# Performance work log

Hardware: AMD Instinct MI355X
Metric: run time of the kernel (lower is better)

## Reference

```python
import jax, jax.numpy as jnp
import numpy as np

N = 100000   # nodes
E = 1600000  # edges (avg degree 16)
IN, HID, OUT = 128, 128, 64
EPS = 1e-5


def setup_inputs() -> dict:
    key = jax.random.key(0)
    ks = jax.random.split(key, 8)
    x = jax.random.normal(ks[0], (N, IN), dtype=jnp.float32)
    edge_index = jax.random.randint(ks[1], (2, E), 0, N, dtype=jnp.int64)

    def w(k, i, o):
        return jax.random.normal(k, (i, o), dtype=jnp.float32) / np.float32(np.sqrt(i))

    return {
        'x': x,
        'edge_index': edge_index,
        'W1': w(ks[2], IN, HID), 'b1': jnp.zeros((HID,), jnp.float32),
        'g1': jnp.ones((HID,), jnp.float32), 'be1': jnp.zeros((HID,), jnp.float32),
        'W2': w(ks[3], HID, HID), 'b2': jnp.zeros((HID,), jnp.float32),
        'g2': jnp.ones((HID,), jnp.float32), 'be2': jnp.zeros((HID,), jnp.float32),
        'W3': w(ks[4], HID, OUT), 'b3': jnp.zeros((OUT,), jnp.float32),
    }


def gcn_conv(x, W, b, src, dst, n):
    # GCNConv: x' = D^{-1/2} (A + I) D^{-1/2} X W + b
    h = x @ W                                   # [N, F_out]
    loop = jnp.arange(n, dtype=src.dtype)
    s = jnp.concatenate([src, loop])            # self-loops appended
    d = jnp.concatenate([dst, loop])
    deg = jax.ops.segment_sum(jnp.ones_like(d, dtype=h.dtype), d, num_segments=n)
    dinv = jax.lax.rsqrt(jnp.maximum(deg, 1.0))  # deg >= 1 due to self-loops
    norm = dinv[s] * dinv[d]                     # [E+N]
    out = jax.ops.segment_sum(h[s] * norm[:, None], d, num_segments=n)
    return out + b


def batch_norm(x, gamma, beta):
    m = x.mean(axis=0)
    v = x.var(axis=0)  # biased variance, as used for normalization in torch BN
    return (x - m) * jax.lax.rsqrt(v + EPS) * gamma + beta


def reference(x, edge_index, W1, b1, g1, be1, W2, b2, g2, be2, W3, b3):
    src, dst = edge_index[0], edge_index[1]
    r = x                                        # residual (skip = Identity, in_dim == hidden_dim)
    h = batch_norm(gcn_conv(x, W1, b1, src, dst, N), g1, be1) + r
    r = h
    h = jax.nn.relu(h)                           # dropout p=0 -> identity
    h = batch_norm(gcn_conv(h, W2, b2, src, dst, N), g2, be2) + r
    h = jax.nn.relu(h)
    out = gcn_conv(h, W3, b3, src, dst, N)       # last layer: no bn/skip/relu
    return out
```

## Files before the change

### kernel.cpp

```cpp
#include <hip/hip_runtime.h>

static constexpr int kN = 100000;
static constexpr int kE = 1600000;
static constexpr float kEps = 1e-5f;

static constexpr int kBSH = 9;
static constexpr int kNB = (kN + 511) >> kBSH;
static constexpr int kBCAP = 12288;
static constexpr int kCHUNK = 4096;
static constexpr int kPad = 16;

typedef __attribute__((ext_vector_type(8))) short short8;
typedef __attribute__((ext_vector_type(4))) float float4v;
typedef __attribute__((ext_vector_type(2))) float float2v;

static __device__ inline unsigned short f2bf(float f) {
  union { float f; unsigned int u; } v; v.f = f;
  unsigned int r = v.u + 0x7fffu + ((v.u >> 16) & 1u);
  return (unsigned short)(r >> 16);
}
static __device__ inline float bf2f(unsigned int bits16) {
  union { unsigned int u; float f; } v; v.u = bits16 << 16; return v.f;
}
static __device__ inline unsigned int pack2bf(float lo, float hi) {
  return (unsigned int)f2bf(lo) | ((unsigned int)f2bf(hi) << 16);
}

__global__ __launch_bounds__(512) void bin_k(const int* __restrict__ src,
                                             const int* __restrict__ dst,
                                             int* __restrict__ gcursor,
                                             int2* __restrict__ gstage) {
  __shared__ int s_cnt[256];
  __shared__ int s_scan[256];
  __shared__ int s_base[256];
  __shared__ int s_cur[256];
  __shared__ int s_gb[256];
  __shared__ int2 s_stage[kCHUNK];
  int tid = threadIdx.x;
  int e0 = blockIdx.x * kCHUNK;
  int n = kE - e0; if (n > kCHUNK) n = kCHUNK;
  if (tid < 256) s_cnt[tid] = 0;
  __syncthreads();
  for (int j = tid; j < n; j += 512) {
    atomicAdd(&s_cnt[dst[e0 + j] >> kBSH], 1);
  }
  __syncthreads();
  int v = 0;
  if (tid < 256) { v = s_cnt[tid]; s_scan[tid] = v; }
  __syncthreads();
  #pragma unroll
  for (int o = 1; o < 256; o <<= 1) {
    int t = (tid >= o && tid < 256) ? s_scan[tid - o] : 0;
    __syncthreads();
    if (tid < 256) s_scan[tid] += t;
    __syncthreads();
  }
  if (tid < 256) {
    int excl = s_scan[tid] - v;
    s_base[tid] = excl;
    s_cur[tid] = excl;
  }
  __syncthreads();
  if (tid < kNB && s_cnt[tid] > 0) s_gb[tid] = atomicAdd(&gcursor[tid], s_cnt[tid]);
  for (int j = tid; j < n; j += 512) {
    int s = src[e0 + j];
    int d = dst[e0 + j];
    int p = atomicAdd(&s_cur[d >> kBSH], 1);
    s_stage[p] = make_int2(s, d);
  }
  __syncthreads();
  for (int j = tid; j < n; j += 512) {
    int2 e = s_stage[j];
    int b = e.y >> kBSH;
    gstage[(size_t)b * kBCAP + s_gb[b] + (j - s_base[b])] = e;
  }
}

__global__ __launch_bounds__(256) void alloc_hist_k(const int2* __restrict__ gstage,
                                                    const int* __restrict__ gcursor,
                                                    int* __restrict__ counter,
                                                    int* __restrict__ deg,
                                                    int* __restrict__ row_start,
                                                    float* __restrict__ dinv) {
  __shared__ int s_deg[1 << kBSH];
  __shared__ int s_scan[256];
  __shared__ int s_bcast;
  int b = blockIdx.x, tid = threadIdx.x;
  int n0 = b << kBSH;
  s_deg[tid] = 0;
  s_deg[tid + 256] = 0;
  __syncthreads();
  int cnt = gcursor[b];
  const int2* seg = gstage + (size_t)b * kBCAP;
  for (int j = tid; j < cnt; j += 256) {
    atomicAdd(&s_deg[seg[j].y - n0], 1);
  }
  __syncthreads();
  int i0 = 2 * tid, i1 = 2 * tid + 1;
  int d0 = s_deg[i0], d1 = s_deg[i1];
  int pd0 = (d0 + kPad - 1) & ~(kPad - 1);
  int pd1 = (d1 + kPad - 1) & ~(kPad - 1);
  int sum = pd0 + pd1;
  s_scan[tid] = sum;
  __syncthreads();
  #pragma unroll
  for (int o = 1; o < 256; o <<= 1) {
    int t = (tid >= o) ? s_scan[tid - o] : 0;
    __syncthreads();
    s_scan[tid] += t;
    __syncthreads();
  }
  if (tid == 255) s_bcast = atomicAdd(counter, s_scan[255]);
  __syncthreads();
  int base = s_bcast + s_scan[tid] - sum;
  int node0 = n0 + i0, node1 = n0 + i1;
  if (node0 < kN) {
    deg[node0] = d0;
    row_start[node0] = base;
    dinv[node0] = rsqrtf((float)(d0 + 1));
  }
  if (node1 < kN) {
    deg[node1] = d1;
    row_start[node1] = base + pd0;
    dinv[node1] = rsqrtf((float)(d1 + 1));
  }
}

__global__ __launch_bounds__(256) void scatter2_k(const int2* __restrict__ gstage,
                                                  const int* __restrict__ gcursor,
                                                  const int* __restrict__ rowst,
                                                  const int* __restrict__ deg,
                                                  int* __restrict__ csr_src) {
  __shared__ int s_cur[1 << kBSH];
  int b = blockIdx.x, tid = threadIdx.x;
  int n0 = b << kBSH;
  int nn = kN - n0; if (nn > (1 << kBSH)) nn = 1 << kBSH;
  for (int i = tid; i < nn; i += 256) s_cur[i] = rowst[n0 + i];
  __syncthreads();
  int cnt = gcursor[b];
  const int2* seg = gstage + (size_t)b * kBCAP;
  for (int j = tid; j < cnt; j += 256) {
    int2 e = seg[j];
    int pos = atomicAdd(&s_cur[e.y - n0], 1);
    csr_src[pos] = e.x;
  }
  __syncthreads();
  for (int i = tid; i < nn; i += 256) {
    int d = deg[n0 + i];
    int endp = rowst[n0 + i] + ((d + kPad - 1) & ~(kPad - 1));
    for (int p = s_cur[i]; p < endp; ++p) csr_src[p] = kN;
  }
}

__global__ void convert_w_all_k(const float* __restrict__ W1, const float* __restrict__ W2,
                                const float* __restrict__ W3,
                                unsigned short* __restrict__ wf1,
                                unsigned short* __restrict__ wf2,
                                unsigned short* __restrict__ wf3,
                                unsigned char* __restrict__ hF8,
                                unsigned short* __restrict__ hH,
                                float* __restrict__ stats) {
  int tid = blockIdx.x * blockDim.x + threadIdx.x;
  const float* W;
  unsigned short* Wf;
  int BNO;
  if (tid < 2048) { W = W1; Wf = wf1; BNO = 128; }
  else if (tid < 4096) { W = W2; Wf = wf2; BNO = 128; tid -= 2048; }
  else if (tid < 5120) { W = W3; Wf = wf3; BNO = 64; tid -= 4096; }
  else if (tid < 5152) {
    ((unsigned int*)(hF8 + (size_t)kN * 128))[tid - 5120] = 0u;
    return;
  } else if (tid < 5184) {
    ((unsigned int*)(hH + (size_t)kN * 64))[tid - 5152] = 0u;
    return;
  } else if (tid < 5696) {
    stats[tid - 5184] = 0.f;
    return;
  } else return;
  int l = tid & 63;
  int frag = tid >> 6;
  int q = frag & 3;
  int t = frag >> 2;
  int n = t * 16 + (l & 15);
  int kbase = q * 32 + ((l >> 4) << 3);
  unsigned short v[8] __attribute__((aligned(16)));
  #pragma unroll
  for (int j = 0; j < 8; ++j) v[j] = f2bf(W[(kbase + j) * BNO + n]);
  ((uint4*)Wf)[tid] = *(const uint4*)v;
}

template <int BNO, int AMODE, bool OUT8>
__global__ __launch_bounds__(256) void gemm_mfma_k(const void* __restrict__ Aptr,
                                                   const void* __restrict__ Rptr,
                                                   const float* __restrict__ stats,
                                                   const float* __restrict__ g,
                                                   const float* __restrict__ be,
                                                   unsigned int* __restrict__ Zptr,
                                                   const unsigned short* __restrict__ Wf,
                                                   const float* __restrict__ dinv,
                                                   void* __restrict__ Cptr) {
  __shared__ float lss[256];
  if constexpr (AMODE != 0) {
    int t = threadIdx.x;
    if (t < 128) {
      float mean = stats[t] * (1.f / kN);
      float var = stats[128 + t] * (1.f / kN) - mean * mean;
      float inv = rsqrtf(var + kEps);
      float sc = g[t] * inv;
      lss[t] = sc;
      lss[128 + t] = be[t] - mean * sc;
    }
    __syncthreads();
  }
  int wid = (int)((blockIdx.x * blockDim.x + threadIdx.x) >> 6);
  if (wid >= kN / 16) return;
  int l = threadIdx.x & 63;
  int r0 = wid * 16;
  short8 a[4];
  if constexpr (AMODE == 0) {
    const float* Af = (const float*)Aptr + (size_t)(r0 + (l & 15)) * 128 + ((l >> 4) << 3);
    #pragma unroll
    for (int q = 0; q < 4; ++q) {
      float4 u0 = *(const float4*)(Af + q * 32);
      float4 u1 = *(const float4*)(Af + q * 32 + 4);
      short8 t;
      t[0] = (short)f2bf(u0.x); t[1] = (short)f2bf(u0.y);
      t[2] = (short)f2bf(u0.z); t[3] = (short)f2bf(u0.w);
      t[4] = (short)f2bf(u1.x); t[5] = (short)f2bf(u1.y);
      t[6] = (short)f2bf(u1.z); t[7] = (short)f2bf(u1.w);
      a[q] = t;
    }
  } else {
    int row = r0 + (l & 15);
    int cg0 = l >> 4;
    const uint4* Ab = (const uint4*)Aptr + (size_t)row * 16;
    #pragma unroll
    for (int q = 0; q < 4; ++q) {
      int cg = q * 4 + cg0;
      int c0 = cg * 8;
      uint4 av = Ab[cg];
      float r[8];
      if constexpr (AMODE == 1) {
        const float4* Rf = (const float4*)Rptr + (size_t)row * 32 + cg * 2;
        float4 r0v = Rf[0], r1v = Rf[1];
        r[0] = r0v.x; r[1] = r0v.y; r[2] = r0v.z; r[3] = r0v.w;
        r[4] = r1v.x; r[5] = r1v.y; r[6] = r1v.z; r[7] = r1v.w;
      } else {
        uint4 rv = ((const uint4*)Rptr)[(size_t)row * 16 + cg];
        r[0] = bf2f(rv.x & 0xffffu); r[1] = bf2f(rv.x >> 16);
        r[2] = bf2f(rv.y & 0xffffu); r[3] = bf2f(rv.y >> 16);
        r[4] = bf2f(rv.z & 0xffffu); r[5] = bf2f(rv.z >> 16);
        r[6] = bf2f(rv.w & 0xffffu); r[7] = bf2f(rv.w >> 16);
      }
      unsigned int apk[4] = {av.x, av.y, av.z, av.w};
      float o[8];
      #pragma unroll
      for (int j = 0; j < 4; ++j) {
        o[2 * j]     = lss[c0 + 2 * j] * bf2f(apk[j] & 0xffffu) + lss[128 + c0 + 2 * j] + r[2 * j];
        o[2 * j + 1] = lss[c0 + 2 * j + 1] * bf2f(apk[j] >> 16) + lss[128 + c0 + 2 * j + 1] + r[2 * j + 1];
      }
      if constexpr (AMODE == 1) {
        uint4 zv;
        zv.x = pack2bf(o[0], o[1]); zv.y = pack2bf(o[2], o[3]);
        zv.z = pack2bf(o[4], o[5]); zv.w = pack2bf(o[6], o[7]);
        ((uint4*)Zptr)[(size_t)row * 16 + cg] = zv;
      }
      short8 t;
      #pragma unroll
      for (int j = 0; j < 8; ++j) t[j] = (short)f2bf(fmaxf(o[j], 0.f));
      a[q] = t;
    }
  }
  const short8* Wv = (const short8*)Wf + l;
  constexpr int NT = BNO / 16;
  float4v acc[NT];
  #pragma unroll
  for (int t = 0; t < NT; ++t) {
    acc[t] = (float4v){0.f, 0.f, 0.f, 0.f};
    #pragma unroll
    for (int q = 0; q < 4; ++q) {
      short8 b = Wv[(t * 4 + q) * 64];
      acc[t] = __builtin_amdgcn_mfma_f32_16x16x32_bf16(a[q], b, acc[t], 0, 0, 0);
    }
  }
  int orow = r0 + ((l >> 4) << 2);
  int ocol = l & 15;
  float dv[4];
  #pragma unroll
  for (int r = 0; r < 4; ++r) dv[r] = dinv[orow + r];
  #pragma unroll
  for (int t = 0; t < NT; ++t) {
    #pragma unroll
    for (int r = 0; r < 4; ++r) {
      float val = acc[t][r] * dv[r];
      if constexpr (OUT8) {
        unsigned int u = __builtin_amdgcn_cvt_pk_fp8_f32(val, val, 0u, false);
        ((unsigned char*)Cptr)[(size_t)(orow + r) * BNO + t * 16 + ocol] = (unsigned char)(u & 0xffu);
      } else {
        ((unsigned short*)Cptr)[(size_t)(orow + r) * BNO + t * 16 + ocol] = f2bf(val);
      }
    }
  }
}

__global__ __launch_bounds__(256) void aggregate128_k(
    const unsigned char* __restrict__ H8, const int* __restrict__ row_start,
    const int* __restrict__ deg, const int* __restrict__ csr_src,
    const float* __restrict__ dinv, const float* __restrict__ bias,
    unsigned int* __restrict__ outp, float* __restrict__ stats) {
  __shared__ float s_sum[128], s_sq[128];
  int tid = threadIdx.x;
  if (tid < 128) { s_sum[tid] = 0.f; s_sq[tid] = 0.f; }
  __syncthreads();
  int lane = tid & 63;
  int qt = lane >> 4;
  int ql = lane & 15;
  int nwaves = gridDim.x * (blockDim.x >> 6);
  int gwave = (int)((blockIdx.x * blockDim.x + tid) >> 6);
  const uint2* H2 = (const uint2*)H8;
  float4 blo = ((const float4*)bias)[2 * ql];
  float4 bhi = ((const float4*)bias)[2 * ql + 1];
  float st[8] = {0.f, 0.f, 0.f, 0.f, 0.f, 0.f, 0.f, 0.f};
  float sqa[8] = {0.f, 0.f, 0.f, 0.f, 0.f, 0.f, 0.f, 0.f};
  auto accum = [](float (&a)[8], uint2 v) {
    float2v p0 = __builtin_amdgcn_cvt_pk_f32_fp8(v.x, false);
    float2v p1 = __builtin_amdgcn_cvt_pk_f32_fp8(v.x, true);
    float2v p2 = __builtin_amdgcn_cvt_pk_f32_fp8(v.y, false);
    float2v p3 = __builtin_amdgcn_cvt_pk_f32_fp8(v.y, true);
    a[0] += p0.x; a[1] += p0.y; a[2] += p1.x; a[3] += p1.y;
    a[4] += p2.x; a[5] += p2.y; a[6] += p3.x; a[7] += p3.y;
  };
  int node = gwave;
  int rs = 0, pd = 0;
  float di = 1.f;
  int ec = kN;
  if (node < kN) {
    rs = row_start[node];
    pd = (deg[node] + kPad - 1) & ~(kPad - 1);
    di = dinv[node];
    ec = csr_src[rs + lane];
  }
  while (node < kN) {
    int cur_rs = rs, cur_pd = pd, cur_e = ec;
    float cur_di = di;
    int nxt = node + nwaves;
    if (nxt < kN) {
      rs = row_start[nxt];
      pd = (deg[nxt] + kPad - 1) & ~(kPad - 1);
      di = dinv[nxt];
      ec = csr_src[rs + lane];
    }
    float a[8] = {0.f, 0.f, 0.f, 0.f, 0.f, 0.f, 0.f, 0.f};
    uint2 vself = H2[(size_t)node * 16 + ql];
    int nb = cur_pd >> 4;
    int nb4 = nb > 4 ? 4 : nb;
    for (int i = 0; i < nb4; ++i) {
      int s[4];
      uint2 v[4];
      #pragma unroll
      for (int j = 0; j < 4; ++j) s[j] = __shfl(cur_e, i * 16 + 4 * j + qt, 64);
      #pragma unroll
      for (int j = 0; j < 4; ++j) v[j] = H2[(size_t)s[j] * 16 + ql];
      #pragma unroll
      for (int j = 0; j < 4; ++j) accum(a, v[j]);
    }
    for (int i = 4; i < nb; ++i) {
      int ee = csr_src[cur_rs + i * 16 + (lane & 15)];
      int s[4];
      uint2 v[4];
      #pragma unroll
      for (int j = 0; j < 4; ++j) s[j] = __shfl(ee, 4 * j + qt, 64);
      #pragma unroll
      for (int j = 0; j < 4; ++j) v[j] = H2[(size_t)s[j] * 16 + ql];
      #pragma unroll
      for (int j = 0; j < 4; ++j) accum(a, v[j]);
    }
    #pragma unroll
    for (int j = 0; j < 8; ++j) {
      a[j] += __shfl_xor(a[j], 16, 64);
      a[j] += __shfl_xor(a[j], 32, 64);
    }
    accum(a, vself);
    if (qt == 0) {
      float o[8];
      o[0] = cur_di * a[0] + blo.x; o[1] = cur_di * a[1] + blo.y;
      o[2] = cur_di * a[2] + blo.z; o[3] = cur_di * a[3] + blo.w;
      o[4] = cur_di * a[4] + bhi.x; o[5] = cur_di * a[5] + bhi.y;
      o[6] = cur_di * a[6] + bhi.z; o[7] = cur_di * a[7] + bhi.w;
      uint4 ov;
      ov.x = pack2bf(o[0], o[1]); ov.y = pack2bf(o[2], o[3]);
      ov.z = pack2bf(o[4], o[5]); ov.w = pack2bf(o[6], o[7]);
      ((uint4*)outp)[(size_t)node * 16 + ql] = ov;
      #pragma unroll
      for (int j = 0; j < 8; ++j) { st[j] += o[j]; sqa[j] += o[j] * o[j]; }
    }
    node = nxt;
  }
  if (qt == 0) {
    #pragma unroll
    for (int j = 0; j < 8; ++j) {
      atomicAdd(&s_sum[8 * ql + j], st[j]);
      atomicAdd(&s_sq[8 * ql + j], sqa[j]);
    }
  }
  __syncthreads();
  if (tid < 128) {
    atomicAdd(&stats[tid], s_sum[tid]);
    atomicAdd(&stats[128 + tid], s_sq[tid]);
  }
}

__global__ __launch_bounds__(256) void aggregate64_k(
    const unsigned short* __restrict__ Hb, const int* __restrict__ row_start,
    const int* __restrict__ deg, const int* __restrict__ csr_src,
    const float* __restrict__ dinv, const float* __restrict__ bias,
    float* __restrict__ outp) {
  int tid = threadIdx.x;
  int lane = tid & 63;
  int qt = lane >> 4;
  int ql = lane & 15;
  int nwaves = gridDim.x * (blockDim.x >> 6);
  int gwave = (int)((blockIdx.x * blockDim.x + tid) >> 6);
  const uint2* H2 = (const uint2*)Hb;
  float4 b4 = ((const float4*)bias)[ql];
  auto accum = [](float (&a)[4], uint2 v) {
    a[0] += bf2f(v.x & 0xffffu); a[1] += bf2f(v.x >> 16);
    a[2] += bf2f(v.y & 0xffffu); a[3] += bf2f(v.y >> 16);
  };
  int node = gwave;
  int rs = 0, pd = 0;
  float di = 1.f;
  int ec = kN;
  if (node < kN) {
    rs = row_start[node];
    pd = (deg[node] + kPad - 1) & ~(kPad - 1);
    di = dinv[node];
    ec = csr_src[rs + lane];
  }
  while (node < kN) {
    int cur_rs = rs, cur_pd = pd, cur_e = ec;
    float cur_di = di;
    int nxt = node + nwaves;
    if (nxt < kN) {
      rs = row_start[nxt];
      pd = (deg[nxt] + kPad - 1) & ~(kPad - 1);
      di = dinv[nxt];
      ec = csr_src[rs + lane];
    }
    float a[4] = {0.f, 0.f, 0.f, 0.f};
    uint2 vself = H2[(size_t)node * 16 + ql];
    int nb = cur_pd >> 4;
    int nb4 = nb > 4 ? 4 : nb;
    for (int i = 0; i < nb4; ++i) {
      int s[4];
      uint2 v[4];
      #pragma unroll
      for (int j = 0; j < 4; ++j) s[j] = __shfl(cur_e, i * 16 + 4 * j + qt, 64);
      #pragma unroll
      for (int j = 0; j < 4; ++j) v[j] = H2[(size_t)s[j] * 16 + ql];
      #pragma unroll
      for (int j = 0; j < 4; ++j) accum(a, v[j]);
    }
    for (int i = 4; i < nb; ++i) {
      int ee = csr_src[cur_rs + i * 16 + (lane & 15)];
      int s[4];
      uint2 v[4];
      #pragma unroll
      for (int j = 0; j < 4; ++j) s[j] = __shfl(ee, 4 * j + qt, 64);
      #pragma unroll
      for (int j = 0; j < 4; ++j) v[j] = H2[(size_t)s[j] * 16 + ql];
      #pragma unroll
      for (int j = 0; j < 4; ++j) accum(a, v[j]);
    }
    #pragma unroll
    for (int j = 0; j < 4; ++j) {
      a[j] += __shfl_xor(a[j], 16, 64);
      a[j] += __shfl_xor(a[j], 32, 64);
    }
    accum(a, vself);
    if (qt == 0) {
      ((float4*)outp)[(size_t)node * 16 + ql] =
          make_float4(cur_di * a[0] + b4.x, cur_di * a[1] + b4.y,
                      cur_di * a[2] + b4.z, cur_di * a[3] + b4.w);
    }
    node = nxt;
  }
}

extern "C" void kernel_launch(void* const* d_in, const int* in_sizes, int n_in,
                              void* d_out, int out_size, void* d_ws, size_t ws_size,
                              hipStream_t stream) {
  const float* x   = (const float*)d_in[0];
  const int*   ei  = (const int*)d_in[1];
  const float* W1  = (const float*)d_in[2];
  const float* b1  = (const float*)d_in[3];
  const float* g1  = (const float*)d_in[4];
  const float* be1 = (const float*)d_in[5];
  const float* W2  = (const float*)d_in[6];
  const float* b2  = (const float*)d_in[7];
  const float* g2  = (const float*)d_in[8];
  const float* be2 = (const float*)d_in[9];
  const float* W3  = (const float*)d_in[10];
  const float* b3  = (const float*)d_in[11];
  float* outp = (float*)d_out;

  const int* src = ei;
  const int* dst = ei + kE;

  char* ws = (char*)d_ws;
  size_t off = 0;
  auto alloc = [&](size_t bytes) -> void* {
    void* p = ws + off;
    off = (off + bytes + 255) & ~size_t(255);
    return p;
  };
  unsigned char* hF8 = (unsigned char*)alloc((size_t)(kN + 1) * 128);
  unsigned short* hH = (unsigned short*)alloc((size_t)(kN + 1) * 64 * 2);
  unsigned int* aB = (unsigned int*)alloc((size_t)kN * 64 * 4);
  unsigned int* zC = (unsigned int*)alloc((size_t)kN * 64 * 4);
  int*   csr_src  = (int*)alloc((size_t)(3200000 + 64) * 4);
  int2*  gstage   = (int2*)alloc((size_t)kNB * kBCAP * 8);
  int*   gcursor  = (int*)alloc((kNB + 1) * 4);
  int*   counter  = gcursor + kNB;
  int*   deg      = (int*)alloc((size_t)kN * 4);
  float* dinv     = (float*)alloc((size_t)kN * 4);
  int*   rowst    = (int*)alloc((size_t)kN * 4);
  float* stats    = (float*)alloc(512 * 4);
  float* statsA   = stats;
  float* statsB   = stats + 256;
  unsigned short* wf1 = (unsigned short*)alloc(128 * 128 * 2);
  unsigned short* wf2 = (unsigned short*)alloc(128 * 128 * 2);
  unsigned short* wf3 = (unsigned short*)alloc(128 * 64 * 2);

  const int TB = 256;
  int blkBin = (kE + kCHUNK - 1) / kCHUNK;
  int blkGemm = (kN / 16 + 3) / 4;
  const int blkAgg = 2048;

  hipMemsetAsync(gcursor, 0, (kNB + 1) * 4, stream);
  bin_k<<<blkBin, 512, 0, stream>>>(src, dst, gcursor, gstage);
  alloc_hist_k<<<kNB, TB, 0, stream>>>(gstage, gcursor, counter, deg, rowst, dinv);
  scatter2_k<<<kNB, TB, 0, stream>>>(gstage, gcursor, rowst, deg, csr_src);
  convert_w_all_k<<<23, TB, 0, stream>>>(W1, W2, W3, wf1, wf2, wf3, hF8, hH, stats);

  gemm_mfma_k<128, 0, true><<<blkGemm, TB, 0, stream>>>(
      x, nullptr, nullptr, nullptr, nullptr, nullptr, wf1, dinv, hF8);
  aggregate128_k<<<blkAgg, TB, 0, stream>>>(hF8, rowst, deg, csr_src, dinv, b1, aB, statsA);

  gemm_mfma_k<128, 1, true><<<blkGemm, TB, 0, stream>>>(
      aB, x, statsA, g1, be1, zC, wf2, dinv, hF8);
  aggregate128_k<<<blkAgg, TB, 0, stream>>>(hF8, rowst, deg, csr_src, dinv, b2, aB, statsB);

  gemm_mfma_k<64, 2, false><<<blkGemm, TB, 0, stream>>>(
      aB, zC, statsB, g2, be2, nullptr, wf3, dinv, hH);
  aggregate64_k<<<blkAgg, TB, 0, stream>>>(hH, rowst, deg, csr_src, dinv, b3, outp);
}
```

Before: 406.7 us.

## Software-pipeline neighbor gathers across nodes in aggregation kernels

Both aggregation kernels now load the first 32 neighbor rows and the self row of the next node while accumulating the current node. Node metadata is loaded two nodes ahead. Out-of-range slots are redirected to the sentinel row kN so the prefetch loads need no branches. The aim is to hide gather latency in this memory-bound stage by keeping more loads in flight. The cost is higher register pressure, which may reduce occupancy, plus wasted loads for low-degree nodes. Bias loads also move inside the store branch.

Result: slower. 452.4 us (+11.2%).

```diff
diff --git a/kernel.cpp b/kernel.cpp
--- a/kernel.cpp
+++ b/kernel.cpp
@@ -318,8 +318,6 @@
   int nwaves = gridDim.x * (blockDim.x >> 6);
   int gwave = (int)((blockIdx.x * blockDim.x + tid) >> 6);
   const uint2* H2 = (const uint2*)H8;
-  float4 blo = ((const float4*)bias)[2 * ql];
-  float4 bhi = ((const float4*)bias)[2 * ql + 1];
   float st[8] = {0.f, 0.f, 0.f, 0.f, 0.f, 0.f, 0.f, 0.f};
   float sqa[8] = {0.f, 0.f, 0.f, 0.f, 0.f, 0.f, 0.f, 0.f};
   auto accum = [](float (&a)[8], uint2 v) {
@@ -330,42 +328,60 @@
     a[0] += p0.x; a[1] += p0.y; a[2] += p1.x; a[3] += p1.y;
     a[4] += p2.x; a[5] += p2.y; a[6] += p3.x; a[7] += p3.y;
   };
-  int node = gwave;
-  int rs = 0, pd = 0;
-  float di = 1.f;
-  int ec = kN;
-  if (node < kN) {
-    rs = row_start[node];
-    pd = (deg[node] + kPad - 1) & ~(kPad - 1);
-    di = dinv[node];
-    ec = csr_src[rs + lane];
-  }
-  while (node < kN) {
-    int cur_rs = rs, cur_pd = pd, cur_e = ec;
-    float cur_di = di;
-    int nxt = node + nwaves;
-    if (nxt < kN) {
-      rs = row_start[nxt];
-      pd = (deg[nxt] + kPad - 1) & ~(kPad - 1);
-      di = dinv[nxt];
+  auto ldmeta = [&](int nd, int& rs, int& pd, float& di, int& ec) {
+    if (nd < kN) {
+      rs = row_start[nd];
+      pd = (deg[nd] + kPad - 1) & ~(kPad - 1);
+      di = dinv[nd];
       ec = csr_src[rs + lane];
-    }
+    } else { rs = 0; pd = 0; di = 1.f; ec = kN; }
+  };
+  auto issue = [&](int nd, int pd, int ec, uint2& vs, uint2 (&g0)[4], uint2 (&g1)[4]) {
+    int ndc = nd < kN ? nd : kN;
+    vs = H2[(size_t)ndc * 16 + ql];
+    #pragma unroll
+    for (int j = 0; j < 4; ++j) {
+      int s = __shfl(ec, 4 * j + qt, 64);
+      s = (pd > 0) ? s : kN;
+      g0[j] = H2[(size_t)s * 16 + ql];
+    }
+    #pragma unroll
+    for (int j = 0; j < 4; ++j) {
+      int s = __shfl(ec, 16 + 4 * j + qt, 64);
+      s = (pd >= 32) ? s : kN;
+      g1[j] = H2[(size_t)s * 16 + ql];
+    }
+  };
+  int n0 = gwave, n1 = gwave + nwaves, n2 = gwave + 2 * nwaves;
+  int rs0, pd0, ec0, rs1, pd1, ec1, rs2, pd2, ec2;
+  float di0, di1, di2;
+  uint2 vs0, g0a[4], g1a[4];
+  ldmeta(n0, rs0, pd0, di0, ec0);
+  ldmeta(n1, rs1, pd1, di1, ec1);
+  issue(n0, pd0, ec0, vs0, g0a, g1a);
+  while (n0 < kN) {
+    ldmeta(n2, rs2, pd2, di2, ec2);
+    uint2 vs1, g0b[4], g1b[4];
+    issue(n1, pd1, ec1, vs1, g0b, g1b);
     float a[8] = {0.f, 0.f, 0.f, 0.f, 0.f, 0.f, 0.f, 0.f};
-    uint2 vself = H2[(size_t)node * 16 + ql];
-    int nb = cur_pd >> 4;
+    #pragma unroll
+    for (int j = 0; j < 4; ++j) accum(a, g0a[j]);
+    #pragma unroll
+    for (int j = 0; j < 4; ++j) accum(a, g1a[j]);
+    int nb = pd0 >> 4;
     int nb4 = nb > 4 ? 4 : nb;
-    for (int i = 0; i < nb4; ++i) {
+    for (int i = 2; i < nb4; ++i) {
       int s[4];
       uint2 v[4];
       #pragma unroll
-      for (int j = 0; j < 4; ++j) s[j] = __shfl(cur_e, i * 16 + 4 * j + qt, 64);
+      for (int j = 0; j < 4; ++j) s[j] = __shfl(ec0, i * 16 + 4 * j + qt, 64);
       #pragma unroll
       for (int j = 0; j < 4; ++j) v[j] = H2[(size_t)s[j] * 16 + ql];
       #pragma unroll
       for (int j = 0; j < 4; ++j) accum(a, v[j]);
     }
     for (int i = 4; i < nb; ++i) {
-      int ee = csr_src[cur_rs + i * 16 + (lane & 15)];
+      int ee = csr_src[rs0 + i * 16 + (lane & 15)];
       int s[4];
       uint2 v[4];
       #pragma unroll
@@ -380,21 +396,27 @@
       a[j] += __shfl_xor(a[j], 16, 64);
       a[j] += __shfl_xor(a[j], 32, 64);
     }
-    accum(a, vself);
+    accum(a, vs0);
     if (qt == 0) {
+      float4 blo = ((const float4*)bias)[2 * ql];
+      float4 bhi = ((const float4*)bias)[2 * ql + 1];
       float o[8];
-      o[0] = cur_di * a[0] + blo.x; o[1] = cur_di * a[1] + blo.y;
-      o[2] = cur_di * a[2] + blo.z; o[3] = cur_di * a[3] + blo.w;
-      o[4] = cur_di * a[4] + bhi.x; o[5] = cur_di * a[5] + bhi.y;
-      o[6] = cur_di * a[6] + bhi.z; o[7] = cur_di * a[7] + bhi.w;
+      o[0] = di0 * a[0] + blo.x; o[1] = di0 * a[1] + blo.y;
+      o[2] = di0 * a[2] + blo.z; o[3] = di0 * a[3] + blo.w;
+      o[4] = di0 * a[4] + bhi.x; o[5] = di0 * a[5] + bhi.y;
+      o[6] = di0 * a[6] + bhi.z; o[7] = di0 * a[7] + bhi.w;
       uint4 ov;
       ov.x = pack2bf(o[0], o[1]); ov.y = pack2bf(o[2], o[3]);
       ov.z = pack2bf(o[4], o[5]); ov.w = pack2bf(o[6], o[7]);
-      ((uint4*)outp)[(size_t)node * 16 + ql] = ov;
+      ((uint4*)outp)[(size_t)n0 * 16 + ql] = ov;
       #pragma unroll
       for (int j = 0; j < 8; ++j) { st[j] += o[j]; sqa[j] += o[j] * o[j]; }
     }
-    node = nxt;
+    n0 = n1; rs0 = rs1; pd0 = pd1; di0 = di1; ec0 = ec1; vs0 = vs1;
+    #pragma unroll
+    for (int j = 0; j < 4; ++j) { g0a[j] = g0b[j]; g1a[j] = g1b[j]; }
+    n1 = n2; rs1 = rs2; pd1 = pd2; di1 = di2; ec1 = ec2;
+    n2 += nwaves;
   }
   if (qt == 0) {
     #pragma unroll
@@ -422,47 +444,64 @@
   int nwaves = gridDim.x * (blockDim.x >> 6);
   int gwave = (int)((blockIdx.x * blockDim.x + tid) >> 6);
   const uint2* H2 = (const uint2*)Hb;
-  float4 b4 = ((const float4*)bias)[ql];
   auto accum = [](float (&a)[4], uint2 v) {
     a[0] += bf2f(v.x & 0xffffu); a[1] += bf2f(v.x >> 16);
     a[2] += bf2f(v.y & 0xffffu); a[3] += bf2f(v.y >> 16);
   };
-  int node = gwave;
-  int rs = 0, pd = 0;
-  float di = 1.f;
-  int ec = kN;
-  if (node < kN) {
-    rs = row_start[node];
-    pd = (deg[node] + kPad - 1) & ~(kPad - 1);
-    di = dinv[node];
-    ec = csr_src[rs + lane];
-  }
-  while (node < kN) {
-    int cur_rs = rs, cur_pd = pd, cur_e = ec;
-    float cur_di = di;
-    int nxt = node + nwaves;
-    if (nxt < kN) {
-      rs = row_start[nxt];
-      pd = (deg[nxt] + kPad - 1) & ~(kPad - 1);
-      di = dinv[nxt];
+  auto ldmeta = [&](int nd, int& rs, int& pd, float& di, int& ec) {
+    if (nd < kN) {
+      rs = row_start[nd];
+      pd = (deg[nd] + kPad - 1) & ~(kPad - 1);
+      di = dinv[nd];
       ec = csr_src[rs + lane];
-    }
+    } else { rs = 0; pd = 0; di = 1.f; ec = kN; }
+  };
+  auto issue = [&](int nd, int pd, int ec, uint2& vs, uint2 (&g0)[4], uint2 (&g1)[4]) {
+    int ndc = nd < kN ? nd : kN;
+    vs = H2[(size_t)ndc * 16 + ql];
+    #pragma unroll
+    for (int j = 0; j < 4; ++j) {
+      int s = __shfl(ec, 4 * j + qt, 64);
+      s = (pd > 0) ? s : kN;
+      g0[j] = H2[(size_t)s * 16 + ql];
+    }
+    #pragma unroll
+    for (int j = 0; j < 4; ++j) {
+      int s = __shfl(ec, 16 + 4 * j + qt, 64);
+      s = (pd >= 32) ? s : kN;
+      g1[j] = H2[(size_t)s * 16 + ql];
+    }
+  };
+  int n0 = gwave, n1 = gwave + nwaves, n2 = gwave + 2 * nwaves;
+  int rs0, pd0, ec0, rs1, pd1, ec1, rs2, pd2, ec2;
+  float di0, di1, di2;
+  uint2 vs0, g0a[4], g1a[4];
+  ldmeta(n0, rs0, pd0, di0, ec0);
+  ldmeta(n1, rs1, pd1, di1, ec1);
+  issue(n0, pd0, ec0, vs0, g0a, g1a);
+  while (n0 < kN) {
+    ldmeta(n2, rs2, pd2, di2, ec2);
+    uint2 vs1, g0b[4], g1b[4];
+    issue(n1, pd1, ec1, vs1, g0b, g1b);
     float a[4] = {0.f, 0.f, 0.f, 0.f};
-    uint2 vself = H2[(size_t)node * 16 + ql];
-    int nb = cur_pd >> 4;
+    #pragma unroll
+    for (int j = 0; j < 4; ++j) accum(a, g0a[j]);
+    #pragma unroll
+    for (int j = 0; j < 4; ++j) accum(a, g1a[j]);
+    int nb = pd0 >> 4;
     int nb4 = nb > 4 ? 4 : nb;
-    for (int i = 0; i < nb4; ++i) {
+    for (int i = 2; i < nb4; ++i) {
       int s[4];
       uint2 v[4];
       #pragma unroll
-      for (int j = 0; j < 4; ++j) s[j] = __shfl(cur_e, i * 16 + 4 * j + qt, 64);
+      for (int j = 0; j < 4; ++j) s[j] = __shfl(ec0, i * 16 + 4 * j + qt, 64);
       #pragma unroll
       for (int j = 0; j < 4; ++j) v[j] = H2[(size_t)s[j] * 16 + ql];
       #pragma unroll
       for (int j = 0; j < 4; ++j) accum(a, v[j]);
     }
     for (int i = 4; i < nb; ++i) {
-      int ee = csr_src[cur_rs + i * 16 + (lane & 15)];
+      int ee = csr_src[rs0 + i * 16 + (lane & 15)];
       int s[4];
       uint2 v[4];
       #pragma unroll
@@ -477,13 +516,18 @@
       a[j] += __shfl_xor(a[j], 16, 64);
       a[j] += __shfl_xor(a[j], 32, 64);
     }
-    accum(a, vself);
+    accum(a, vs0);
     if (qt == 0) {
-      ((float4*)outp)[(size_t)node * 16 + ql] =
-          make_float4(cur_di * a[0] + b4.x, cur_di * a[1] + b4.y,
-                      cur_di * a[2] + b4.z, cur_di * a[3] + b4.w);
-    }
-    node = nxt;
+      float4 b4 = ((const float4*)bias)[ql];
+      ((float4*)outp)[(size_t)n0 * 16 + ql] =
+          make_float4(di0 * a[0] + b4.x, di0 * a[1] + b4.y,
+                      di0 * a[2] + b4.z, di0 * a[3] + b4.w);
+    }
+    n0 = n1; rs0 = rs1; pd0 = pd1; di0 = di1; ec0 = ec1; vs0 = vs1;
+    #pragma unroll
+    for (int j = 0; j < 4; ++j) { g0a[j] = g0b[j]; g1a[j] = g1b[j]; }
+    n1 = n2; rs1 = rs2; pd1 = pd2; di1 = di2; ec1 = ec2;
+    n2 += nwaves;
   }
 }
 
```

## Fuse CSR alloc and scatter kernels, vectorize edge binning, drop memset

Applied to the files above, without the earlier changes.

Merges the degree-histogram/row-allocation kernel with the CSR scatter kernel so row starts and row ends stay in shared memory instead of being written out and read back. The edge-binning kernel now reads src/dst as int4 vectors. The gcursor memset is folded into the weight-conversion kernel, which now runs first. Together these remove one launch and a memset. The int4 loops assume the edge chunk length is a multiple of four, which holds for E=1.6M.

Result: no change. 400.2 us (-1.6%).

```diff
diff --git a/kernel.cpp b/kernel.cpp
--- a/kernel.cpp
+++ b/kernel.cpp
@@ -39,10 +39,17 @@
   int tid = threadIdx.x;
   int e0 = blockIdx.x * kCHUNK;
   int n = kE - e0; if (n > kCHUNK) n = kCHUNK;
+  int n4 = n >> 2;
   if (tid < 256) s_cnt[tid] = 0;
   __syncthreads();
-  for (int j = tid; j < n; j += 512) {
-    atomicAdd(&s_cnt[dst[e0 + j] >> kBSH], 1);
+  const int4* d4p = (const int4*)(dst + e0);
+  const int4* s4p = (const int4*)(src + e0);
+  for (int j = tid; j < n4; j += 512) {
+    int4 d4 = d4p[j];
+    atomicAdd(&s_cnt[d4.x >> kBSH], 1);
+    atomicAdd(&s_cnt[d4.y >> kBSH], 1);
+    atomicAdd(&s_cnt[d4.z >> kBSH], 1);
+    atomicAdd(&s_cnt[d4.w >> kBSH], 1);
   }
   __syncthreads();
   int v = 0;
@@ -62,11 +69,14 @@
   }
   __syncthreads();
   if (tid < kNB && s_cnt[tid] > 0) s_gb[tid] = atomicAdd(&gcursor[tid], s_cnt[tid]);
-  for (int j = tid; j < n; j += 512) {
-    int s = src[e0 + j];
-    int d = dst[e0 + j];
-    int p = atomicAdd(&s_cur[d >> kBSH], 1);
-    s_stage[p] = make_int2(s, d);
+  for (int j = tid; j < n4; j += 512) {
+    int4 s4 = s4p[j];
+    int4 d4 = d4p[j];
+    int p;
+    p = atomicAdd(&s_cur[d4.x >> kBSH], 1); s_stage[p] = make_int2(s4.x, d4.x);
+    p = atomicAdd(&s_cur[d4.y >> kBSH], 1); s_stage[p] = make_int2(s4.y, d4.y);
+    p = atomicAdd(&s_cur[d4.z >> kBSH], 1); s_stage[p] = make_int2(s4.z, d4.z);
+    p = atomicAdd(&s_cur[d4.w >> kBSH], 1); s_stage[p] = make_int2(s4.w, d4.w);
   }
   __syncthreads();
   for (int j = tid; j < n; j += 512) {
@@ -76,14 +86,17 @@
   }
 }
 
-__global__ __launch_bounds__(256) void alloc_hist_k(const int2* __restrict__ gstage,
-                                                    const int* __restrict__ gcursor,
-                                                    int* __restrict__ counter,
-                                                    int* __restrict__ deg,
-                                                    int* __restrict__ row_start,
-                                                    float* __restrict__ dinv) {
+__global__ __launch_bounds__(256) void alloc_scatter_k(const int2* __restrict__ gstage,
+                                                       const int* __restrict__ gcursor,
+                                                       int* __restrict__ counter,
+                                                       int* __restrict__ deg,
+                                                       int* __restrict__ row_start,
+                                                       float* __restrict__ dinv,
+                                                       int* __restrict__ csr_src) {
   __shared__ int s_deg[1 << kBSH];
   __shared__ int s_scan[256];
+  __shared__ int s_rs[1 << kBSH];
+  __shared__ int s_end[1 << kBSH];
   __shared__ int s_bcast;
   int b = blockIdx.x, tid = threadIdx.x;
   int n0 = b << kBSH;
@@ -124,31 +137,21 @@
     row_start[node1] = base + pd0;
     dinv[node1] = rsqrtf((float)(d1 + 1));
   }
-}
-
-__global__ __launch_bounds__(256) void scatter2_k(const int2* __restrict__ gstage,
-                                                  const int* __restrict__ gcursor,
-                                                  const int* __restrict__ rowst,
-                                                  const int* __restrict__ deg,
-                                                  int* __restrict__ csr_src) {
-  __shared__ int s_cur[1 << kBSH];
-  int b = blockIdx.x, tid = threadIdx.x;
-  int n0 = b << kBSH;
-  int nn = kN - n0; if (nn > (1 << kBSH)) nn = 1 << kBSH;
-  for (int i = tid; i < nn; i += 256) s_cur[i] = rowst[n0 + i];
-  __syncthreads();
-  int cnt = gcursor[b];
-  const int2* seg = gstage + (size_t)b * kBCAP;
+  s_rs[i0] = base;
+  s_rs[i1] = base + pd0;
+  s_end[i0] = base + pd0;
+  s_end[i1] = base + pd0 + pd1;
+  __syncthreads();
   for (int j = tid; j < cnt; j += 256) {
     int2 e = seg[j];
-    int pos = atomicAdd(&s_cur[e.y - n0], 1);
+    int pos = atomicAdd(&s_rs[e.y - n0], 1);
     csr_src[pos] = e.x;
   }
   __syncthreads();
+  int nn = kN - n0; if (nn > (1 << kBSH)) nn = 1 << kBSH;
   for (int i = tid; i < nn; i += 256) {
-    int d = deg[n0 + i];
-    int endp = rowst[n0 + i] + ((d + kPad - 1) & ~(kPad - 1));
-    for (int p = s_cur[i]; p < endp; ++p) csr_src[p] = kN;
+    int endp = s_end[i];
+    for (int p = s_rs[i]; p < endp; ++p) csr_src[p] = kN;
   }
 }
 
@@ -159,7 +162,8 @@
                                 unsigned short* __restrict__ wf3,
                                 unsigned char* __restrict__ hF8,
                                 unsigned short* __restrict__ hH,
-                                float* __restrict__ stats) {
+                                float* __restrict__ stats,
+                                int* __restrict__ gcursor) {
   int tid = blockIdx.x * blockDim.x + threadIdx.x;
   const float* W;
   unsigned short* Wf;
@@ -175,6 +179,9 @@
     return;
   } else if (tid < 5696) {
     stats[tid - 5184] = 0.f;
+    return;
+  } else if (tid < 5696 + kNB + 1) {
+    gcursor[tid - 5696] = 0;
     return;
   } else return;
   int l = tid & 63;
@@ -537,11 +544,9 @@
   int blkGemm = (kN / 16 + 3) / 4;
   const int blkAgg = 2048;
 
-  hipMemsetAsync(gcursor, 0, (kNB + 1) * 4, stream);
+  convert_w_all_k<<<24, TB, 0, stream>>>(W1, W2, W3, wf1, wf2, wf3, hF8, hH, stats, gcursor);
   bin_k<<<blkBin, 512, 0, stream>>>(src, dst, gcursor, gstage);
-  alloc_hist_k<<<kNB, TB, 0, stream>>>(gstage, gcursor, counter, deg, rowst, dinv);
-  scatter2_k<<<kNB, TB, 0, stream>>>(gstage, gcursor, rowst, deg, csr_src);
-  convert_w_all_k<<<23, TB, 0, stream>>>(W1, W2, W3, wf1, wf2, wf3, hF8, hH, stats);
+  alloc_scatter_k<<<kNB, TB, 0, stream>>>(gstage, gcursor, counter, deg, rowst, dinv, csr_src);
 
   gemm_mfma_k<128, 0, true><<<blkGemm, TB, 0, stream>>>(
       x, nullptr, nullptr, nullptr, nullptr, nullptr, wf1, dinv, hF8);
```
